# Kernel optimization log

Hardware: AMD Instinct MI355X
Metric: run time of the kernel (lower is better)

## Reference

```python
import jax, jax.numpy as jnp
import numpy as np

EPS = 1e-5

def setup_inputs() -> dict:
    key = jax.random.key(0)
    ks = jax.random.split(key, 10)
    B, S, C, Q, D = 16, 2048, 768, 1024, 64
    clamp3_features = jax.random.normal(ks[0], (B, S, C), dtype=jnp.float32)
    residual = jax.random.normal(ks[1], (B, S, Q), dtype=jnp.float32)
    # params (xavier-ish scale; up-proj given small random values instead of zeros
    # so the output is non-trivial for correctness testing)
    Wproj = jax.random.normal(ks[2], (Q, C), dtype=jnp.float32) * (1.0 / np.sqrt(C))
    Wdown = jax.random.normal(ks[3], (D, Q), dtype=jnp.float32) * (1.0 / np.sqrt(Q))
    gamma = jnp.ones((D,), dtype=jnp.float32)
    beta = jnp.zeros((D,), dtype=jnp.float32)
    Wl1 = jax.random.normal(ks[4], (D, D), dtype=jnp.float32) * (1.0 / np.sqrt(D))
    bl1 = jnp.zeros((D,), dtype=jnp.float32)
    Wl2 = jax.random.normal(ks[5], (D, D), dtype=jnp.float32) * (1.0 / np.sqrt(D))
    bl2 = jnp.zeros((D,), dtype=jnp.float32)
    Wup = jax.random.normal(ks[6], (Q, D), dtype=jnp.float32) * (1.0 / np.sqrt(D))
    return {"clamp3_features": clamp3_features, "residual": residual,
            "Wproj": Wproj, "Wdown": Wdown, "gamma": gamma, "beta": beta,
            "Wl1": Wl1, "bl1": bl1, "Wl2": Wl2, "bl2": bl2, "Wup": Wup}

def _layernorm(x, gamma, beta):
    mu = jnp.mean(x, axis=-1, keepdims=True)
    var = jnp.mean(jnp.square(x - mu), axis=-1, keepdims=True)
    return (x - mu) * jax.lax.rsqrt(var + EPS) * gamma + beta

def reference(clamp3_features, residual, Wproj, Wdown, gamma, beta, Wl1, bl1, Wl2, bl2, Wup):
    # projection (no bias) -> down (no bias) -> LayerNorm
    projected = jnp.einsum('bsc,qc->bsq', clamp3_features, Wproj)
    down = jnp.einsum('bsq,dq->bsd', projected, Wdown)
    normed = _layernorm(down, gamma, beta)
    # SwiGLU: swish(l1(x)) * l2(x)
    o1 = jnp.einsum('bsd,ed->bse', normed, Wl1) + bl1
    swish = o1 * jax.nn.sigmoid(o1)
    gate = jnp.einsum('bsd,ed->bse', normed, Wl2) + bl2
    activated = swish * gate  # dropout is identity in eval mode
    up = jnp.einsum('bsd,qd->bsq', activated, Wup)
    return residual + up
```

## Files before the change

kernel.cpp:

```cpp
#include <hip/hip_runtime.h>


#define CDIM 768
#define QDIM 1024

typedef __attribute__((ext_vector_type(8))) short bf16x8;
typedef __attribute__((ext_vector_type(4))) float f32x4;

__device__ __forceinline__ ushort f2bf(float f) {
  union { float f; unsigned u; } v; v.f = f;
  unsigned r = v.u + 0x7fffu + ((v.u >> 16) & 1u);
  return (ushort)(r >> 16);
}

__global__ void k_wcomb(const float* __restrict__ Wproj, const float* __restrict__ Wdown,
                        float* __restrict__ part) {
  int bid = blockIdx.x;
  int cb = bid % 12, db = (bid / 12) % 8, qc = bid / 96;
  int l = threadIdx.x;
  int c = cb * 64 + l;
  float acc[8];
  #pragma unroll
  for (int i = 0; i < 8; ++i) acc[i] = 0.f;
  int q0 = qc * 128;
  for (int q = q0; q < q0 + 128; ++q) {
    float xp = Wproj[q * CDIM + c];
    #pragma unroll
    for (int i = 0; i < 8; ++i)
      acc[i] = fmaf(Wdown[(db * 8 + i) * QDIM + q], xp, acc[i]);
  }
  #pragma unroll
  for (int i = 0; i < 8; ++i)
    part[((size_t)qc * CDIM + c) * 64 + db * 8 + i] = acc[i];
}

__global__ void k_arrange(const float* __restrict__ part, const float* __restrict__ Wup,
                          const float* __restrict__ Wl1, const float* __restrict__ Wl2,
                          ushort* __restrict__ wcf, ushort* __restrict__ wupf,
                          ushort* __restrict__ wl1f, ushort* __restrict__ wl2f) {
  int idx = blockIdx.x * 256 + threadIdx.x;
  if (idx < 49152) {
    int i0 = idx;
    int j = i0 & 7, l = (i0 >> 3) & 63, t = i0 >> 9;
    int g = l >> 4, r16 = l & 15;
    int nf = t & 3, ks = t >> 2;
    int k = 32 * ks + 8 * g + j, n = 16 * nf + r16;
    float s = 0.f;
    #pragma unroll
    for (int qc = 0; qc < 8; ++qc) s += part[((size_t)qc * CDIM + k) * 64 + n];
    wcf[i0] = f2bf(s);
  } else if (idx < 49152 + 65536) {
    int i2 = idx - 49152;
    int j = i2 & 7, l = (i2 >> 3) & 63, t = i2 >> 9;
    int g = l >> 4, r16 = l & 15;
    int ks = t & 1, nf = t >> 1;
    int k = 32 * ks + 8 * g + j, n = 16 * nf + r16;
    wupf[i2] = f2bf(Wup[n * 64 + k]);
  } else if (idx < 49152 + 65536 + 4096) {
    int i3 = idx - (49152 + 65536);
    int j = i3 & 7, l = (i3 >> 3) & 63, t = i3 >> 9;
    int g = l >> 4, r16 = l & 15;
    int nf = t & 3, ks = t >> 2;
    int k = 32 * ks + 8 * g + j, e = 16 * nf + r16;
    wl1f[i3] = f2bf(Wl1[e * 64 + k]);
  } else {
    int i4 = idx - (49152 + 65536 + 4096);
    int j = i4 & 7, l = (i4 >> 3) & 63, t = i4 >> 9;
    int g = l >> 4, r16 = l & 15;
    int nf = t & 3, ks = t >> 2;
    int k = 32 * ks + 8 * g + j, e = 16 * nf + r16;
    wl2f[i4] = f2bf(Wl2[e * 64 + k]);
  }
}

__global__ __launch_bounds__(256, 3)
void k_main(const float* __restrict__ xg, const float* __restrict__ resg,
            const float* __restrict__ gamma, const float* __restrict__ beta,
            const float* __restrict__ bl1, const float* __restrict__ bl2,
            const ushort* __restrict__ wcf, const ushort* __restrict__ wupf,
            const ushort* __restrict__ wl1f, const ushort* __restrict__ wl2f,
            float* __restrict__ outg) {
  __shared__ ushort smem[12416];
  ushort (*x_lds)[776] = reinterpret_cast<ushort(*)[776]>(smem);
  float  (*d_lds)[68]  = reinterpret_cast<float (*)[68]>(smem);
  ushort (*n_lds)[72]  = reinterpret_cast<ushort(*)[72]>(reinterpret_cast<char*>(smem) + 4608);
  ushort (*a_lds)[72]  = reinterpret_cast<ushort(*)[72]>(reinterpret_cast<char*>(smem) + 8192);

  const int tid = threadIdx.x;
  const int w = tid >> 6, l = tid & 63, g = l >> 4, r16 = l & 15;
  const int row0 = blockIdx.x * 16;

  float4 xv[12];
  #pragma unroll
  for (int i = 0; i < 12; ++i) {
    int f4 = i * 256 + tid;
    int r = f4 / 192;
    int c4 = (f4 - r * 192) * 4;
    xv[i] = *reinterpret_cast<const float4*>(xg + (size_t)(row0 + r) * CDIM + c4);
  }
  #pragma unroll
  for (int i = 0; i < 12; ++i) {
    int f4 = i * 256 + tid;
    int r = f4 / 192;
    int c4 = (f4 - r * 192) * 4;
    ushort4 b;
    b.x = f2bf(xv[i].x); b.y = f2bf(xv[i].y); b.z = f2bf(xv[i].z); b.w = f2bf(xv[i].w);
    *reinterpret_cast<ushort4*>(&x_lds[r][c4]) = b;
  }

  const float* rbase = resg + (size_t)(row0 + r16) * QDIM + 256 * w + 4 * g;
  f32x4 rv[16];
  #pragma unroll
  for (int nfl = 0; nfl < 16; ++nfl)
    rv[nfl] = *reinterpret_cast<const f32x4*>(rbase + 16 * nfl);
  #pragma unroll
  for (int nfl = 0; nfl < 16; ++nfl)
    asm volatile("" : "+v"(rv[nfl]));
  __builtin_amdgcn_sched_barrier(0);

  __syncthreads();

  f32x4 dacc = {0.f, 0.f, 0.f, 0.f};
  #pragma unroll 4
  for (int ks = 0; ks < 24; ++ks) {
    bf16x8 a = *reinterpret_cast<const bf16x8*>(&x_lds[r16][ks * 32 + 8 * g]);
    bf16x8 b = *reinterpret_cast<const bf16x8*>(wcf + ((size_t)(ks * 4 + w) * 64 + l) * 8);
    dacc = __builtin_amdgcn_mfma_f32_16x16x32_bf16(a, b, dacc, 0, 0, 0);
  }
  __syncthreads();
  #pragma unroll
  for (int rg = 0; rg < 4; ++rg) d_lds[4 * g + rg][16 * w + r16] = dacc[rg];
  __syncthreads();

  {
    int row = 4 * w + g;
    f32x4 v = *reinterpret_cast<const f32x4*>(&d_lds[row][4 * r16]);
    float s  = v[0] + v[1] + v[2] + v[3];
    float sq = v[0]*v[0] + v[1]*v[1] + v[2]*v[2] + v[3]*v[3];
    #pragma unroll
    for (int m = 1; m < 16; m <<= 1) {
      s  += __shfl_xor(s, m, 64);
      sq += __shfl_xor(sq, m, 64);
    }
    float mu  = s * (1.f / 64.f);
    float var = sq * (1.f / 64.f) - mu * mu;
    float rs  = rsqrtf(var + 1e-5f);
    const float4 gm = *reinterpret_cast<const float4*>(gamma + 4 * r16);
    const float4 bt = *reinterpret_cast<const float4*>(beta  + 4 * r16);
    ushort4 nb;
    nb.x = f2bf((v[0] - mu) * rs * gm.x + bt.x);
    nb.y = f2bf((v[1] - mu) * rs * gm.y + bt.y);
    nb.z = f2bf((v[2] - mu) * rs * gm.z + bt.z);
    nb.w = f2bf((v[3] - mu) * rs * gm.w + bt.w);
    *reinterpret_cast<ushort4*>(&n_lds[row][4 * r16]) = nb;
  }
  __syncthreads();

  {
    bf16x8 a0 = *reinterpret_cast<const bf16x8*>(&n_lds[r16][8 * g]);
    bf16x8 a1 = *reinterpret_cast<const bf16x8*>(&n_lds[r16][32 + 8 * g]);
    bf16x8 b10 = *reinterpret_cast<const bf16x8*>(wl1f + ((size_t)(0 * 4 + w) * 64 + l) * 8);
    bf16x8 b11 = *reinterpret_cast<const bf16x8*>(wl1f + ((size_t)(1 * 4 + w) * 64 + l) * 8);
    bf16x8 b20 = *reinterpret_cast<const bf16x8*>(wl2f + ((size_t)(0 * 4 + w) * 64 + l) * 8);
    bf16x8 b21 = *reinterpret_cast<const bf16x8*>(wl2f + ((size_t)(1 * 4 + w) * 64 + l) * 8);
    f32x4 z = {0.f, 0.f, 0.f, 0.f};
    f32x4 acc1 = __builtin_amdgcn_mfma_f32_16x16x32_bf16(a0, b10, z, 0, 0, 0);
    acc1 = __builtin_amdgcn_mfma_f32_16x16x32_bf16(a1, b11, acc1, 0, 0, 0);
    f32x4 acc2 = __builtin_amdgcn_mfma_f32_16x16x32_bf16(a0, b20, z, 0, 0, 0);
    acc2 = __builtin_amdgcn_mfma_f32_16x16x32_bf16(a1, b21, acc2, 0, 0, 0);
    float bv1 = bl1[16 * w + r16];
    float bv2 = bl2[16 * w + r16];
    #pragma unroll
    for (int rg = 0; rg < 4; ++rg) {
      float o1 = acc1[rg] + bv1;
      float o2 = acc2[rg] + bv2;
      float sw = o1 / (1.f + __expf(-o1));
      a_lds[4 * g + rg][16 * w + r16] = f2bf(sw * o2);
    }
  }
  __syncthreads();

  {
    const bf16x8 af0 = *reinterpret_cast<const bf16x8*>(&a_lds[r16][8 * g]);
    const bf16x8 af1 = *reinterpret_cast<const bf16x8*>(&a_lds[r16][32 + 8 * g]);
    float* obase = outg + (size_t)(row0 + r16) * QDIM + 256 * w + 4 * g;
    #pragma unroll
    for (int nfl = 0; nfl < 16; ++nfl) {
      size_t nf = 16 * w + nfl;
      bf16x8 b0 = *reinterpret_cast<const bf16x8*>(wupf + ((nf * 2 + 0) * 64 + l) * 8);
      bf16x8 b1 = *reinterpret_cast<const bf16x8*>(wupf + ((nf * 2 + 1) * 64 + l) * 8);
      f32x4 t = {0.f, 0.f, 0.f, 0.f};
      t = __builtin_amdgcn_mfma_f32_16x16x32_bf16(b0, af0, t, 0, 0, 0);
      t = __builtin_amdgcn_mfma_f32_16x16x32_bf16(b1, af1, t, 0, 0, 0);
      f32x4 o = rv[nfl] + t;
      *reinterpret_cast<f32x4*>(obase + 16 * nfl) = o;
    }
  }
}

extern "C" void kernel_launch(void* const* d_in, const int* in_sizes, int n_in,
                              void* d_out, int out_size, void* d_ws, size_t ws_size,
                              hipStream_t stream) {
  (void)in_sizes; (void)n_in; (void)out_size; (void)ws_size;
  const float* x     = (const float*)d_in[0];
  const float* resid = (const float*)d_in[1];
  const float* Wproj = (const float*)d_in[2];
  const float* Wdown = (const float*)d_in[3];
  const float* gamma = (const float*)d_in[4];
  const float* beta  = (const float*)d_in[5];
  const float* Wl1   = (const float*)d_in[6];
  const float* bl1   = (const float*)d_in[7];
  const float* Wl2   = (const float*)d_in[8];
  const float* bl2   = (const float*)d_in[9];
  const float* Wup   = (const float*)d_in[10];
  float* out = (float*)d_out;

  char* ws = (char*)d_ws;
  float*  part = (float*)(ws);
  ushort* wcf  = (ushort*)(ws + 1572864);
  ushort* wupf = (ushort*)(ws + 1671168);
  ushort* wl1f = (ushort*)(ws + 1802240);
  ushort* wl2f = (ushort*)(ws + 1810432);

  k_wcomb  <<<768, 64, 0, stream>>>(Wproj, Wdown, part);
  k_arrange<<<480, 256, 0, stream>>>(part, Wup, Wl1, Wl2, wcf, wupf, wl1f, wl2f);
  k_main   <<<2048, 256, 0, stream>>>(x, resid, gamma, beta, bl1, bl2,
                                      wcf, wupf, wl1f, wl2f, out);
}
```

Baseline: 121.0 us.

## Stage residual through LDS with async global_load_lds in two swizzled halves

The residual tile now goes straight to LDS through global_load_lds instead of being held in 64 VGPRs. It is loaded in two 512-column halves with an XOR swizzle, and the second half is issued into the freed x_lds region after the SwiGLU stage. LDS grows to 64KB per block, occupancy drops from 3 to 2 blocks, and the up-projection is split into two phases, each waiting on its half with vmcnt and a barrier. This removes register pressure and overlaps residual loading with compute, at the cost of lower occupancy and extra LDS traffic.

```diff
diff --git a/kernel.cpp b/kernel.cpp
--- a/kernel.cpp
+++ b/kernel.cpp
@@ -6,11 +6,19 @@
 
 typedef __attribute__((ext_vector_type(8))) short bf16x8;
 typedef __attribute__((ext_vector_type(4))) float f32x4;
+
+#define SCHED0() __builtin_amdgcn_sched_barrier(0)
 
 __device__ __forceinline__ ushort f2bf(float f) {
   union { float f; unsigned u; } v; v.f = f;
   unsigned r = v.u + 0x7fffu + ((v.u >> 16) & 1u);
   return (ushort)(r >> 16);
+}
+
+__device__ __forceinline__ void gload16(const float* g, void* lds) {
+  __builtin_amdgcn_global_load_lds(
+      (const __attribute__((address_space(1))) void*)g,
+      (__attribute__((address_space(3))) void*)lds, 16, 0, 0);
 }
 
 __global__ void k_wcomb(const float* __restrict__ Wproj, const float* __restrict__ Wdown,
@@ -73,61 +81,55 @@
   }
 }
 
-__global__ __launch_bounds__(256, 3)
+template<int DUMMY>
+__global__ __launch_bounds__(256, 2)
 void k_main(const float* __restrict__ xg, const float* __restrict__ resg,
             const float* __restrict__ gamma, const float* __restrict__ beta,
             const float* __restrict__ bl1, const float* __restrict__ bl2,
             const ushort* __restrict__ wcf, const ushort* __restrict__ wupf,
             const ushort* __restrict__ wl1f, const ushort* __restrict__ wl2f,
             float* __restrict__ outg) {
-  __shared__ ushort smem[12416];
+  __shared__ alignas(16) char smem[65536];
   ushort (*x_lds)[776] = reinterpret_cast<ushort(*)[776]>(smem);
-  float  (*d_lds)[68]  = reinterpret_cast<float (*)[68]>(smem);
-  ushort (*n_lds)[72]  = reinterpret_cast<ushort(*)[72]>(reinterpret_cast<char*>(smem) + 4608);
-  ushort (*a_lds)[72]  = reinterpret_cast<ushort(*)[72]>(reinterpret_cast<char*>(smem) + 8192);
+  float  (*d_lds)[68]  = reinterpret_cast<float (*)[68]>(smem + 24832);
+  ushort (*a_lds)[72]  = reinterpret_cast<ushort(*)[72]>(smem + 24832);
+  ushort (*n_lds)[72]  = reinterpret_cast<ushort(*)[72]>(smem + 29184);
+  float* r1 = reinterpret_cast<float*>(smem);
+  float* r0 = reinterpret_cast<float*>(smem + 32768);
 
   const int tid = threadIdx.x;
   const int w = tid >> 6, l = tid & 63, g = l >> 4, r16 = l & 15;
   const int row0 = blockIdx.x * 16;
-
-  float4 xv[12];
+  const size_t rrow = (size_t)row0 * QDIM;
+
+  #pragma unroll
+  for (int s = 0; s < 8; ++s) {
+    int G = s * 256 + tid;
+    int r = G >> 7, p = G & 127;
+    gload16(resg + rrow + (size_t)r * QDIM + 4 * (p ^ (r & 7)),
+            smem + 32768 + (size_t)(s * 256 + w * 64) * 16);
+  }
+  SCHED0();
+
   #pragma unroll
   for (int i = 0; i < 12; ++i) {
     int f4 = i * 256 + tid;
     int r = f4 / 192;
     int c4 = (f4 - r * 192) * 4;
-    xv[i] = *reinterpret_cast<const float4*>(xg + (size_t)(row0 + r) * CDIM + c4);
-  }
-  #pragma unroll
-  for (int i = 0; i < 12; ++i) {
-    int f4 = i * 256 + tid;
-    int r = f4 / 192;
-    int c4 = (f4 - r * 192) * 4;
+    const float4 v = *reinterpret_cast<const float4*>(xg + (size_t)(row0 + r) * CDIM + c4);
     ushort4 b;
-    b.x = f2bf(xv[i].x); b.y = f2bf(xv[i].y); b.z = f2bf(xv[i].z); b.w = f2bf(xv[i].w);
+    b.x = f2bf(v.x); b.y = f2bf(v.y); b.z = f2bf(v.z); b.w = f2bf(v.w);
     *reinterpret_cast<ushort4*>(&x_lds[r][c4]) = b;
   }
-
-  const float* rbase = resg + (size_t)(row0 + r16) * QDIM + 256 * w + 4 * g;
-  f32x4 rv[16];
-  #pragma unroll
-  for (int nfl = 0; nfl < 16; ++nfl)
-    rv[nfl] = *reinterpret_cast<const f32x4*>(rbase + 16 * nfl);
-  #pragma unroll
-  for (int nfl = 0; nfl < 16; ++nfl)
-    asm volatile("" : "+v"(rv[nfl]));
-  __builtin_amdgcn_sched_barrier(0);
-
   __syncthreads();
 
   f32x4 dacc = {0.f, 0.f, 0.f, 0.f};
-  #pragma unroll 4
+  #pragma unroll 8
   for (int ks = 0; ks < 24; ++ks) {
     bf16x8 a = *reinterpret_cast<const bf16x8*>(&x_lds[r16][ks * 32 + 8 * g]);
     bf16x8 b = *reinterpret_cast<const bf16x8*>(wcf + ((size_t)(ks * 4 + w) * 64 + l) * 8);
     dacc = __builtin_amdgcn_mfma_f32_16x16x32_bf16(a, b, dacc, 0, 0, 0);
   }
-  __syncthreads();
   #pragma unroll
   for (int rg = 0; rg < 4; ++rg) d_lds[4 * g + rg][16 * w + r16] = dacc[rg];
   __syncthreads();
@@ -180,20 +182,58 @@
   }
   __syncthreads();
 
-  {
-    const bf16x8 af0 = *reinterpret_cast<const bf16x8*>(&a_lds[r16][8 * g]);
-    const bf16x8 af1 = *reinterpret_cast<const bf16x8*>(&a_lds[r16][32 + 8 * g]);
-    float* obase = outg + (size_t)(row0 + r16) * QDIM + 256 * w + 4 * g;
-    #pragma unroll
-    for (int nfl = 0; nfl < 16; ++nfl) {
-      size_t nf = 16 * w + nfl;
+  const bf16x8 af0 = *reinterpret_cast<const bf16x8*>(&a_lds[r16][8 * g]);
+  const bf16x8 af1 = *reinterpret_cast<const bf16x8*>(&a_lds[r16][32 + 8 * g]);
+  asm volatile("s_waitcnt lgkmcnt(0)" ::: "memory");
+  SCHED0();
+  __builtin_amdgcn_s_barrier();
+  SCHED0();
+
+  #pragma unroll
+  for (int s = 0; s < 8; ++s) {
+    int G = s * 256 + tid;
+    int r = G >> 7, p = G & 127;
+    gload16(resg + rrow + (size_t)r * QDIM + 512 + 4 * (p ^ (r & 7)),
+            smem + (size_t)(s * 256 + w * 64) * 16);
+  }
+  SCHED0();
+
+  {
+    float* obase = outg + rrow + (size_t)r16 * QDIM + 128 * w + 4 * g;
+    const float* rb = r0 + r16 * 512;
+    #pragma unroll
+    for (int i = 0; i < 8; ++i) {
+      size_t nf = 8 * w + i;
       bf16x8 b0 = *reinterpret_cast<const bf16x8*>(wupf + ((nf * 2 + 0) * 64 + l) * 8);
       bf16x8 b1 = *reinterpret_cast<const bf16x8*>(wupf + ((nf * 2 + 1) * 64 + l) * 8);
       f32x4 t = {0.f, 0.f, 0.f, 0.f};
       t = __builtin_amdgcn_mfma_f32_16x16x32_bf16(b0, af0, t, 0, 0, 0);
       t = __builtin_amdgcn_mfma_f32_16x16x32_bf16(b1, af1, t, 0, 0, 0);
-      f32x4 o = rv[nfl] + t;
-      *reinterpret_cast<f32x4*>(obase + 16 * nfl) = o;
+      int p = (32 * w + 4 * i + g) ^ (r16 & 7);
+      f32x4 rv = *reinterpret_cast<const f32x4*>(rb + 4 * p);
+      *reinterpret_cast<f32x4*>(obase + 16 * i) = rv + t;
+    }
+  }
+  SCHED0();
+  asm volatile("s_waitcnt vmcnt(8)" ::: "memory");
+  SCHED0();
+  __builtin_amdgcn_s_barrier();
+  SCHED0();
+
+  {
+    float* obase = outg + rrow + (size_t)r16 * QDIM + 512 + 128 * w + 4 * g;
+    const float* rb = r1 + r16 * 512;
+    #pragma unroll
+    for (int i = 0; i < 8; ++i) {
+      size_t nf = 32 + 8 * w + i;
+      bf16x8 b0 = *reinterpret_cast<const bf16x8*>(wupf + ((nf * 2 + 0) * 64 + l) * 8);
+      bf16x8 b1 = *reinterpret_cast<const bf16x8*>(wupf + ((nf * 2 + 1) * 64 + l) * 8);
+      f32x4 t = {0.f, 0.f, 0.f, 0.f};
+      t = __builtin_amdgcn_mfma_f32_16x16x32_bf16(b0, af0, t, 0, 0, 0);
+      t = __builtin_amdgcn_mfma_f32_16x16x32_bf16(b1, af1, t, 0, 0, 0);
+      int p = (32 * w + 4 * i + g) ^ (r16 & 7);
+      f32x4 rv = *reinterpret_cast<const f32x4*>(rb + 4 * p);
+      *reinterpret_cast<f32x4*>(obase + 16 * i) = rv + t;
     }
   }
 }
@@ -224,6 +264,6 @@
 
   k_wcomb  <<<768, 64, 0, stream>>>(Wproj, Wdown, part);
   k_arrange<<<480, 256, 0, stream>>>(part, Wup, Wl1, Wl2, wcf, wupf, wl1f, wl2f);
-  k_main   <<<2048, 256, 0, stream>>>(x, resid, gamma, beta, bl1, bl2,
+  k_main<0><<<2048, 256, 0, stream>>>(x, resid, gamma, beta, bl1, bl2,
                                       wcf, wupf, wl1f, wl2f, out);
 }
```

Measured after the change: 129.4 us. 6.9% more time.
